# Optimization experiments

Hardware: AMD Instinct MI355X
Metric: run time of the kernel (lower is better)

Reference implementation:

```python
import jax, jax.numpy as jnp
import numpy as np

B, N, E, ENT, D, H, L = 64, 2048, 32768, 100000, 256, 256, 512


def setup_inputs() -> dict:
    key = jax.random.key(0)
    ks = jax.random.split(key, 12)
    return {
        "neighbors": jax.random.randint(ks[0], (B, N), 0, ENT),
        "adj_row": jax.random.randint(ks[1], (B, E), 0, N),
        "adj_col": jax.random.randint(ks[2], (B, E), 0, N),
        "adj_val": jax.random.uniform(ks[3], (B, E), dtype=jnp.float32),
        "emb_table": jax.random.normal(ks[4], (ENT, D), dtype=jnp.float32),
        "W1": jax.random.normal(ks[5], (D, H), dtype=jnp.float32) * (1.0 / np.sqrt(H)),
        "b1": jax.random.normal(ks[6], (H,), dtype=jnp.float32) * 0.01,
        "W2": jax.random.normal(ks[7], (H, H), dtype=jnp.float32) * (1.0 / np.sqrt(H)),
        "b2": jax.random.normal(ks[8], (H,), dtype=jnp.float32) * 0.01,
        "fc1_w": jax.random.normal(ks[9], (H, H), dtype=jnp.float32) * (1.0 / np.sqrt(H)),
        "fc1_b": jax.random.normal(ks[10], (H,), dtype=jnp.float32) * 0.01,
        "cur_len": L,
    }


def _gcn_layer(x, W, b, adj_row, adj_col, adj_val):
    # x: [B,N,din] -> support: [B,N,dout]
    support = jnp.einsum("bnd,dh->bnh", x, W)
    # sparse adj @ support: gather columns, scale by edge value, scatter-add to rows
    gathered = jnp.take_along_axis(support, adj_col[:, :, None], axis=1)  # [B,E,h]
    weighted = gathered * adj_val[:, :, None]
    agg = jax.vmap(lambda r, g: jax.ops.segment_sum(g, r, num_segments=N))(adj_row, weighted)
    return agg + b


def reference(neighbors, adj_row, adj_col, adj_val, emb_table, W1, b1, W2, b2, fc1_w, fc1_b, cur_len):
    x = emb_table[neighbors]                                   # [B,N,D] embedding gather
    x = _gcn_layer(x, W1, b1, adj_row, adj_col, adj_val)       # GCN layer 1
    x = _gcn_layer(x, W2, b2, adj_row, adj_col, adj_val)       # GCN layer 2
    seq = x[:, :cur_len, :]                                    # keep cur_node prefix, padded to common L
    pooled = jnp.mean(seq, axis=1, keepdims=True)              # self.seq == 'mean'
    return jax.nn.relu(jnp.einsum("blh,ho->blo", pooled, fc1_w) + fc1_b)  # [B,1,H]
```

## Files before the change

### kernel.cpp

```cpp
#include <hip/hip_runtime.h>

#define B 64
#define N 2048
#define E 32768
#define D 256
#define H 256
#define CH 32
#define SEG 8
#define EPB (E / SEG)

__global__ __launch_bounds__(512) void edge_w_kernel(
    const int* __restrict__ adj_row, const int* __restrict__ adj_col,
    const float* __restrict__ adj_val, const int* __restrict__ cur_len,
    float* __restrict__ w_part)
{
    __shared__ float wloc[N];
    const int b = blockIdx.x, seg = blockIdx.y, tid = threadIdx.x;
    const int L = *cur_len;

    for (int i = tid; i < N; i += 512) wloc[i] = 0.f;
    __syncthreads();

    const int base = b * E + seg * EPB;
    #pragma unroll
    for (int k = 0; k < EPB / 512; ++k) {
        const int e = base + tid + k * 512;
        const int r = adj_row[e];
        if (r < L) atomicAdd(&wloc[adj_col[e]], adj_val[e]);
    }
    __syncthreads();

    float4* dst = (float4*)(w_part + ((size_t)b * SEG + seg) * N);
    const float4* src = (const float4*)wloc;
    dst[tid] = src[tid];
}

__global__ __launch_bounds__(512) void edge_z_kernel(
    const int* __restrict__ adj_row, const int* __restrict__ adj_col,
    const float* __restrict__ adj_val, const float* __restrict__ w_part,
    float* __restrict__ z_part, float* __restrict__ sw_out)
{
    __shared__ float wfull[N];
    __shared__ float zloc[N];
    __shared__ float sred[8];
    const int b = blockIdx.x, seg = blockIdx.y, tid = threadIdx.x;

    float swp = 0.f;
    for (int i = tid; i < N; i += 512) {
        float s = 0.f;
        #pragma unroll
        for (int sg = 0; sg < SEG; ++sg)
            s += w_part[((size_t)b * SEG + sg) * N + i];
        wfull[i] = s;
        zloc[i] = 0.f;
        swp += s;
    }
    __syncthreads();

    if (seg == 0) {
        for (int off = 32; off; off >>= 1) swp += __shfl_down(swp, off, 64);
        if ((tid & 63) == 0) sred[tid >> 6] = swp;
    }
    __syncthreads();
    if (seg == 0 && tid == 0) {
        float s = 0.f;
        #pragma unroll
        for (int i = 0; i < 8; ++i) s += sred[i];
        sw_out[b] = s;
    }

    const int base = b * E + seg * EPB;
    #pragma unroll
    for (int k = 0; k < EPB / 512; ++k) {
        const int e = base + tid + k * 512;
        const float wv = wfull[adj_row[e]];
        if (wv != 0.f) atomicAdd(&zloc[adj_col[e]], wv * adj_val[e]);
    }
    __syncthreads();

    float4* dst = (float4*)(z_part + ((size_t)b * SEG + seg) * N);
    const float4* src = (const float4*)zloc;
    dst[tid] = src[tid];
}

__global__ __launch_bounds__(256) void gather_kernel(
    const int* __restrict__ neighbors, const float* __restrict__ emb,
    const float* __restrict__ z_part, float* __restrict__ u_part)
{
    const int b = blockIdx.x, chunk = blockIdx.y, tid = threadIdx.x;
    const int lane = tid & 63, rg = tid >> 6;
    const int n0 = chunk * (N / CH);

    __shared__ float zs[N / CH];
    __shared__ int   ns[N / CH];
    if (tid < N / CH) {
        float s = 0.f;
        #pragma unroll
        for (int sg = 0; sg < SEG; ++sg)
            s += z_part[((size_t)b * SEG + sg) * N + n0 + tid];
        zs[tid] = s;
        ns[tid] = neighbors[(size_t)b * N + n0 + tid];
    }
    __syncthreads();

    const float4* __restrict__ emb4 = (const float4*)emb;
    float4 a0 = make_float4(0.f,0.f,0.f,0.f), a1 = a0, a2 = a0, a3 = a0;

    #pragma unroll
    for (int i = 0; i < 16; ++i) {
        const int j = i * 4 + rg;
        const float zv = zs[j];
        const size_t idx = (size_t)ns[j];
        const float4 v = emb4[idx * (D / 4) + lane];
        if ((i & 3) == 0)      { a0.x += zv*v.x; a0.y += zv*v.y; a0.z += zv*v.z; a0.w += zv*v.w; }
        else if ((i & 3) == 1) { a1.x += zv*v.x; a1.y += zv*v.y; a1.z += zv*v.z; a1.w += zv*v.w; }
        else if ((i & 3) == 2) { a2.x += zv*v.x; a2.y += zv*v.y; a2.z += zv*v.z; a2.w += zv*v.w; }
        else                   { a3.x += zv*v.x; a3.y += zv*v.y; a3.z += zv*v.z; a3.w += zv*v.w; }
    }
    float4 acc = make_float4(a0.x+a1.x+a2.x+a3.x, a0.y+a1.y+a2.y+a3.y,
                             a0.z+a1.z+a2.z+a3.z, a0.w+a1.w+a2.w+a3.w);

    __shared__ float4 red[256];
    red[tid] = acc;
    __syncthreads();
    if (tid < 64) {
        float4 a = red[tid], bb = red[tid + 64], c = red[tid + 128], d = red[tid + 192];
        float4 s = make_float4(a.x + bb.x + c.x + d.x, a.y + bb.y + c.y + d.y,
                               a.z + bb.z + c.z + d.z, a.w + bb.w + c.w + d.w);
        ((float4*)u_part)[((size_t)b * CH + chunk) * (D / 4) + tid] = s;
    }
}

__global__ __launch_bounds__(1024) void head_kernel(
    const float* __restrict__ u_part, const float* __restrict__ sw,
    const float* __restrict__ W1, const float* __restrict__ b1,
    const float* __restrict__ W2, const float* __restrict__ b2,
    const float* __restrict__ fc1_w, const float* __restrict__ fc1_b,
    const int* __restrict__ cur_len, float* __restrict__ out)
{
    const int b = blockIdx.x;
    const int t = threadIdx.x & 255;
    const int s = threadIdx.x >> 8;
    __shared__ float red[4][256];
    __shared__ float su[D];
    __shared__ float sy[H];
    __shared__ float sp[H];

    float part = 0.f;
    #pragma unroll
    for (int c = 0; c < 8; ++c)
        part += u_part[((size_t)b * CH + s * 8 + c) * D + t];
    red[s][t] = part;
    __syncthreads();
    if (s == 0) su[t] = red[0][t] + red[1][t] + red[2][t] + red[3][t];
    __syncthreads();

    part = 0.f;
    #pragma unroll 8
    for (int k = 0; k < 64; ++k) {
        const int d = s * 64 + k;
        part += su[d] * W1[d * H + t];
    }
    red[s][t] = part;
    __syncthreads();
    if (s == 0) sy[t] = red[0][t] + red[1][t] + red[2][t] + red[3][t] + sw[b] * b1[t];
    __syncthreads();

    const float invL = 1.f / (float)(*cur_len);
    part = 0.f;
    #pragma unroll 8
    for (int k = 0; k < 64; ++k) {
        const int d = s * 64 + k;
        part += sy[d] * W2[d * H + t];
    }
    red[s][t] = part;
    __syncthreads();
    if (s == 0)
        sp[t] = (red[0][t] + red[1][t] + red[2][t] + red[3][t]) * invL + b2[t];
    __syncthreads();

    part = 0.f;
    #pragma unroll 8
    for (int k = 0; k < 64; ++k) {
        const int d = s * 64 + k;
        part += sp[d] * fc1_w[d * H + t];
    }
    red[s][t] = part;
    __syncthreads();
    if (s == 0) {
        const float v = red[0][t] + red[1][t] + red[2][t] + red[3][t] + fc1_b[t];
        out[(size_t)b * H + t] = fmaxf(v, 0.f);
    }
}

extern "C" void kernel_launch(void* const* d_in, const int* in_sizes, int n_in,
                              void* d_out, int out_size, void* d_ws, size_t ws_size,
                              hipStream_t stream) {
    const int*   neighbors = (const int*)  d_in[0];
    const int*   adj_row   = (const int*)  d_in[1];
    const int*   adj_col   = (const int*)  d_in[2];
    const float* adj_val   = (const float*)d_in[3];
    const float* emb_table = (const float*)d_in[4];
    const float* W1        = (const float*)d_in[5];
    const float* b1        = (const float*)d_in[6];
    const float* W2        = (const float*)d_in[7];
    const float* b2        = (const float*)d_in[8];
    const float* fc1_w     = (const float*)d_in[9];
    const float* fc1_b     = (const float*)d_in[10];
    const int*   cur_len   = (const int*)  d_in[11];
    float*       out       = (float*)d_out;

    float* wp_ws = (float*)d_ws;
    float* zp_ws = wp_ws + (size_t)B * SEG * N;
    float* sw_ws = zp_ws + (size_t)B * SEG * N;
    float* u_ws  = sw_ws + 64;

    edge_w_kernel<<<dim3(B, SEG), 512, 0, stream>>>(adj_row, adj_col, adj_val,
                                                    cur_len, wp_ws);
    edge_z_kernel<<<dim3(B, SEG), 512, 0, stream>>>(adj_row, adj_col, adj_val,
                                                    wp_ws, zp_ws, sw_ws);
    gather_kernel<<<dim3(B, CH), 256, 0, stream>>>(neighbors, emb_table, zp_ws, u_ws);
    head_kernel<<<B, 1024, 0, stream>>>(u_ws, sw_ws, W1, b1, W2, b2,
                                        fc1_w, fc1_b, cur_len, out);
}
```

Before: 227.0 us.

## Split partial-w reduction into its own kernel and double edge segments

Edge segments per batch go from 8 to 16 and block size from 512 to 256, giving more, smaller blocks for the shared-memory atomic passes. The summation of w partials, which every edge_z block used to redo, moves into a separate w_reduce kernel that writes w and per-quarter sums once, so edge_z blocks just load the reduced vector. The gather kernel splits the z-partial sum across two thread halves to absorb the larger segment count. This adds a kernel launch and more partial traffic in exchange for less redundant reduction work and higher parallelism.

```diff
diff --git a/kernel.cpp b/kernel.cpp
--- a/kernel.cpp
+++ b/kernel.cpp
@@ -6,10 +6,10 @@
 #define D 256
 #define H 256
 #define CH 32
-#define SEG 8
+#define SEG 16
 #define EPB (E / SEG)
 
-__global__ __launch_bounds__(512) void edge_w_kernel(
+__global__ __launch_bounds__(256) void edge_w_kernel(
     const int* __restrict__ adj_row, const int* __restrict__ adj_col,
     const float* __restrict__ adj_val, const int* __restrict__ cur_len,
     float* __restrict__ w_part)
@@ -18,69 +18,75 @@
     const int b = blockIdx.x, seg = blockIdx.y, tid = threadIdx.x;
     const int L = *cur_len;
 
-    for (int i = tid; i < N; i += 512) wloc[i] = 0.f;
+    ((float4*)wloc)[tid]       = make_float4(0.f, 0.f, 0.f, 0.f);
+    ((float4*)wloc)[tid + 256] = make_float4(0.f, 0.f, 0.f, 0.f);
     __syncthreads();
 
     const int base = b * E + seg * EPB;
     #pragma unroll
-    for (int k = 0; k < EPB / 512; ++k) {
-        const int e = base + tid + k * 512;
+    for (int k = 0; k < EPB / 256; ++k) {
+        const int e = base + tid + k * 256;
         const int r = adj_row[e];
         if (r < L) atomicAdd(&wloc[adj_col[e]], adj_val[e]);
     }
     __syncthreads();
 
     float4* dst = (float4*)(w_part + ((size_t)b * SEG + seg) * N);
-    const float4* src = (const float4*)wloc;
-    dst[tid] = src[tid];
-}
-
-__global__ __launch_bounds__(512) void edge_z_kernel(
-    const int* __restrict__ adj_row, const int* __restrict__ adj_col,
-    const float* __restrict__ adj_val, const float* __restrict__ w_part,
-    float* __restrict__ z_part, float* __restrict__ sw_out)
-{
-    __shared__ float wfull[N];
-    __shared__ float zloc[N];
-    __shared__ float sred[8];
-    const int b = blockIdx.x, seg = blockIdx.y, tid = threadIdx.x;
-
+    dst[tid]       = ((const float4*)wloc)[tid];
+    dst[tid + 256] = ((const float4*)wloc)[tid + 256];
+}
+
+__global__ __launch_bounds__(256) void w_reduce_kernel(
+    const float* __restrict__ w_part, float* __restrict__ w,
+    float* __restrict__ sw_part)
+{
+    __shared__ float sred[4];
+    const int b = blockIdx.x, q = blockIdx.y, tid = threadIdx.x;
     float swp = 0.f;
-    for (int i = tid; i < N; i += 512) {
+    #pragma unroll
+    for (int k = 0; k < 2; ++k) {
+        const int n = q * 512 + k * 256 + tid;
         float s = 0.f;
         #pragma unroll
         for (int sg = 0; sg < SEG; ++sg)
-            s += w_part[((size_t)b * SEG + sg) * N + i];
-        wfull[i] = s;
-        zloc[i] = 0.f;
+            s += w_part[((size_t)b * SEG + sg) * N + n];
+        w[(size_t)b * N + n] = s;
         swp += s;
     }
-    __syncthreads();
-
-    if (seg == 0) {
-        for (int off = 32; off; off >>= 1) swp += __shfl_down(swp, off, 64);
-        if ((tid & 63) == 0) sred[tid >> 6] = swp;
-    }
-    __syncthreads();
-    if (seg == 0 && tid == 0) {
-        float s = 0.f;
-        #pragma unroll
-        for (int i = 0; i < 8; ++i) s += sred[i];
-        sw_out[b] = s;
-    }
+    for (int off = 32; off; off >>= 1) swp += __shfl_down(swp, off, 64);
+    if ((tid & 63) == 0) sred[tid >> 6] = swp;
+    __syncthreads();
+    if (tid == 0) sw_part[b * 4 + q] = sred[0] + sred[1] + sred[2] + sred[3];
+}
+
+__global__ __launch_bounds__(256) void edge_z_kernel(
+    const int* __restrict__ adj_row, const int* __restrict__ adj_col,
+    const float* __restrict__ adj_val, const float* __restrict__ w,
+    float* __restrict__ z_part)
+{
+    __shared__ float wfull[N];
+    __shared__ float zloc[N];
+    const int b = blockIdx.x, seg = blockIdx.y, tid = threadIdx.x;
+
+    const float4* wsrc = (const float4*)(w + (size_t)b * N);
+    ((float4*)wfull)[tid]       = wsrc[tid];
+    ((float4*)wfull)[tid + 256] = wsrc[tid + 256];
+    ((float4*)zloc)[tid]        = make_float4(0.f, 0.f, 0.f, 0.f);
+    ((float4*)zloc)[tid + 256]  = make_float4(0.f, 0.f, 0.f, 0.f);
+    __syncthreads();
 
     const int base = b * E + seg * EPB;
     #pragma unroll
-    for (int k = 0; k < EPB / 512; ++k) {
-        const int e = base + tid + k * 512;
+    for (int k = 0; k < EPB / 256; ++k) {
+        const int e = base + tid + k * 256;
         const float wv = wfull[adj_row[e]];
         if (wv != 0.f) atomicAdd(&zloc[adj_col[e]], wv * adj_val[e]);
     }
     __syncthreads();
 
     float4* dst = (float4*)(z_part + ((size_t)b * SEG + seg) * N);
-    const float4* src = (const float4*)zloc;
-    dst[tid] = src[tid];
+    dst[tid]       = ((const float4*)zloc)[tid];
+    dst[tid + 256] = ((const float4*)zloc)[tid + 256];
 }
 
 __global__ __launch_bounds__(256) void gather_kernel(
@@ -91,15 +97,16 @@
     const int lane = tid & 63, rg = tid >> 6;
     const int n0 = chunk * (N / CH);
 
-    __shared__ float zs[N / CH];
+    __shared__ float zh[2][N / CH];
     __shared__ int   ns[N / CH];
-    if (tid < N / CH) {
+    if (tid < 128) {
+        const int j = tid & 63, half = tid >> 6;
         float s = 0.f;
         #pragma unroll
-        for (int sg = 0; sg < SEG; ++sg)
-            s += z_part[((size_t)b * SEG + sg) * N + n0 + tid];
-        zs[tid] = s;
-        ns[tid] = neighbors[(size_t)b * N + n0 + tid];
+        for (int sg = 0; sg < SEG / 2; ++sg)
+            s += z_part[((size_t)b * SEG + half * (SEG / 2) + sg) * N + n0 + j];
+        zh[half][j] = s;
+        if (half == 0) ns[j] = neighbors[(size_t)b * N + n0 + j];
     }
     __syncthreads();
 
@@ -109,7 +116,7 @@
     #pragma unroll
     for (int i = 0; i < 16; ++i) {
         const int j = i * 4 + rg;
-        const float zv = zs[j];
+        const float zv = zh[0][j] + zh[1][j];
         const size_t idx = (size_t)ns[j];
         const float4 v = emb4[idx * (D / 4) + lane];
         if ((i & 3) == 0)      { a0.x += zv*v.x; a0.y += zv*v.y; a0.z += zv*v.z; a0.w += zv*v.w; }
@@ -132,7 +139,7 @@
 }
 
 __global__ __launch_bounds__(1024) void head_kernel(
-    const float* __restrict__ u_part, const float* __restrict__ sw,
+    const float* __restrict__ u_part, const float* __restrict__ sw_part,
     const float* __restrict__ W1, const float* __restrict__ b1,
     const float* __restrict__ W2, const float* __restrict__ b2,
     const float* __restrict__ fc1_w, const float* __restrict__ fc1_b,
@@ -163,7 +170,11 @@
     }
     red[s][t] = part;
     __syncthreads();
-    if (s == 0) sy[t] = red[0][t] + red[1][t] + red[2][t] + red[3][t] + sw[b] * b1[t];
+    if (s == 0) {
+        const float sw = sw_part[b * 4] + sw_part[b * 4 + 1]
+                       + sw_part[b * 4 + 2] + sw_part[b * 4 + 3];
+        sy[t] = red[0][t] + red[1][t] + red[2][t] + red[3][t] + sw * b1[t];
+    }
     __syncthreads();
 
     const float invL = 1.f / (float)(*cur_len);
@@ -212,13 +223,15 @@
 
     float* wp_ws = (float*)d_ws;
     float* zp_ws = wp_ws + (size_t)B * SEG * N;
-    float* sw_ws = zp_ws + (size_t)B * SEG * N;
-    float* u_ws  = sw_ws + 64;
-
-    edge_w_kernel<<<dim3(B, SEG), 512, 0, stream>>>(adj_row, adj_col, adj_val,
+    float* w_ws  = zp_ws + (size_t)B * SEG * N;
+    float* sw_ws = w_ws  + (size_t)B * N;
+    float* u_ws  = sw_ws + 256;
+
+    edge_w_kernel<<<dim3(B, SEG), 256, 0, stream>>>(adj_row, adj_col, adj_val,
                                                     cur_len, wp_ws);
-    edge_z_kernel<<<dim3(B, SEG), 512, 0, stream>>>(adj_row, adj_col, adj_val,
-                                                    wp_ws, zp_ws, sw_ws);
+    w_reduce_kernel<<<dim3(B, 4), 256, 0, stream>>>(wp_ws, w_ws, sw_ws);
+    edge_z_kernel<<<dim3(B, SEG), 256, 0, stream>>>(adj_row, adj_col, adj_val,
+                                                    w_ws, zp_ws);
     gather_kernel<<<dim3(B, CH), 256, 0, stream>>>(neighbors, emb_table, zp_ws, u_ws);
     head_kernel<<<B, 1024, 0, stream>>>(u_ws, sw_ws, W1, b1, W2, b2,
                                         fc1_w, fc1_b, cur_len, out);
```

New measurement: 231.6 us. +2.0%, slower.
